# Optimization experiments

Hardware: AMD Instinct MI355X
Metric: run time of the kernel (lower is better)

The kernel has to match this reference:

```python
import jax, jax.numpy as jnp
import numpy as np

H = 1024   # longformer-large hidden size
D = 256    # transformer d_model / args.hidden_dim
Q = 100    # num_queries / num_slots
N = 1024   # document length (unpadded tokens)
L = 30     # args.max_span_length
WD = 20    # span width embedding dim
S = N * L - L * (L - 1) // 2  # 30285 candidate spans


def _ln(x, g, b, eps=1e-5):
    m = jnp.mean(x, -1, keepdims=True)
    v = jnp.mean((x - m) ** 2, -1, keepdims=True)
    return (x - m) * jax.lax.rsqrt(v + eps) * g + b


def setup_inputs():
    ks = jax.random.split(jax.random.key(0), 16)
    # deterministic span enumeration: triu(0) & tril(L-1) mention mask, row-major
    idx = np.arange(N)
    m = (idx[None, :] >= idx[:, None]) & (idx[None, :] < idx[:, None] + L)
    ss, ee = np.nonzero(m)
    assert ss.shape[0] == S
    r = lambda i, shape, s=0.02: jax.random.normal(ks[i], shape, jnp.float32) * s
    z = lambda *shape: jnp.zeros(shape, jnp.float32)
    o = lambda *shape: jnp.ones(shape, jnp.float32)
    return dict(
        encoded_doc=jax.random.normal(ks[0], (1, N, H), jnp.float32),
        span_starts=jnp.asarray(ss, jnp.int32),
        span_ends=jnp.asarray(ee, jnp.int32),
        w_word_attn=r(1, (H, 1)), b_word_attn=z(1),
        span_width_embed=r(2, (L, WD)),
        w_span_proj=r(3, (3 * H + WD, D)), b_span_proj=z(D),
        slots_query=r(4, (Q, D)),
        wq=r(5, (D, D)), bq=z(D),
        wk=r(6, (D, D)), bk=z(D),
        wv=r(7, (D, D)), bv=z(D),
        w_ih=r(8, (3 * D, D)), w_hh=r(9, (3 * D, D)), b_ih=z(3 * D), b_hh=z(3 * D),
        w_mlp1=r(10, (D, 2 * D)), b_mlp1=z(2 * D),
        w_mlp2=r(11, (2 * D, D)), b_mlp2=z(D),
        g_in=o(D), beta_in=z(D),
        g_sl=o(D), beta_sl=z(D),
        g_ff=o(D), beta_ff=z(D),
    )


def reference(encoded_doc, span_starts, span_ends, w_word_attn, b_word_attn,
              span_width_embed, w_span_proj, b_span_proj, slots_query,
              wq, bq, wk, bk, wv, bv, w_ih, w_hh, b_ih, b_hh,
              w_mlp1, b_mlp1, w_mlp2, b_mlp2,
              g_in, beta_in, g_sl, beta_sl, g_ff, beta_ff):
    doc = encoded_doc[0]                                   # [N, H]
    # --- get_span_emb ---
    start_emb = doc[span_starts]                           # [S, H]
    end_emb = doc[span_ends]                               # [S, H]
    width_idx = jnp.minimum(1 + span_ends - span_starts, L) - 1
    width_emb = span_width_embed[width_idx]                # [S, WD]
    word_attn = (doc @ w_word_attn)[:, 0] + b_word_attn[0] # [N]
    pos = jnp.arange(N)
    smask = (pos[None, :] >= span_starts[:, None]) & (pos[None, :] <= span_ends[:, None])
    scores = jnp.where(smask, word_attn[None, :], -jnp.inf)  # log(mask)+attn
    head = jax.nn.softmax(scores, axis=-1) @ doc           # [S, H]
    span_emb = jnp.concatenate([start_emb, end_emb, width_emb, head], -1)[None]  # [1,S,3H+WD]
    x = span_emb @ w_span_proj + b_span_proj               # [1, S, D]
    # --- slot attention ---
    inputs = _ln(x, g_in, beta_in)
    k = inputs @ wk + bk
    v = inputs @ wv + bv
    scale = D ** -0.5
    eps = 1e-8
    slots = slots_query[None]                              # [1, Q, D]
    for _ in range(3):
        slots_prev = slots
        q = _ln(slots, g_sl, beta_sl) @ wq + bq
        dots = jnp.einsum('bid,bjd->bij', q, k) * scale    # [1, Q, S]
        attn = jax.nn.softmax(dots, axis=1) + eps          # softmax over slots!
        attn = attn / jnp.sum(attn, -1, keepdims=True)
        updates = jnp.einsum('bjd,bij->bid', v, attn)      # [1, Q, D]
        # torch GRUCell
        xg = updates.reshape(-1, D)
        h = slots_prev.reshape(-1, D)
        gi = xg @ w_ih.T + b_ih
        gh = h @ w_hh.T + b_hh
        ir, iz, inn = jnp.split(gi, 3, -1)
        hr, hz, hn = jnp.split(gh, 3, -1)
        rg = jax.nn.sigmoid(ir + hr)
        zg = jax.nn.sigmoid(iz + hz)
        ng = jnp.tanh(inn + rg * hn)
        slots = ((1.0 - zg) * ng + zg * h).reshape(1, -1, D)
        ff = _ln(slots, g_ff, beta_ff)
        slots = slots + jax.nn.relu(ff @ w_mlp1 + b_mlp1) @ w_mlp2 + b_mlp2
    q = _ln(slots, g_sl, beta_sl) @ wq + bq
    dots = jnp.einsum('bid,bjd->bij', q, k) * scale
    coref_logits = jnp.minimum(jax.nn.softmax(dots, axis=1) + eps, 1.0)  # [1, Q, S]
    return coref_logits, inputs
```

## Files before the change

kernel.cpp:

```cpp
#include <hip/hip_runtime.h>

#define S_TOT 30285
#define SPAD  30720
#define EPS_S 3.0285e-4f

typedef __attribute__((ext_vector_type(8))) short bf16x8;
typedef __attribute__((ext_vector_type(4))) float f32x4;

__device__ __forceinline__ unsigned short f2bf(float f) {
  unsigned u = __float_as_uint(f);
  u += 0x7FFFu + ((u >> 16) & 1u);
  return (unsigned short)(u >> 16);
}
__device__ __forceinline__ float bf2f(unsigned short h) {
  return __uint_as_float(((unsigned)h) << 16);
}
__device__ __forceinline__ float allred_sum(float v) {
#pragma unroll
  for (int o = 32; o > 0; o >>= 1) v += __shfl_xor(v, o, 64);
  return v;
}

__global__ void k_prep(const float* __restrict__ doc, const float* __restrict__ w_wa,
                       const float* __restrict__ b_wa, const float* __restrict__ wemb,
                       const float* __restrict__ wsp, const float* __restrict__ wk,
                       const float* __restrict__ wv, const float* __restrict__ wq,
                       const float* __restrict__ w1, const float* __restrict__ w2,
                       const float* __restrict__ wih, const float* __restrict__ whh,
                       const float* __restrict__ slots_q, float* __restrict__ wa,
                       float* __restrict__ Wd, unsigned short* __restrict__ docb,
                       unsigned short* __restrict__ wihb, unsigned short* __restrict__ whhb,
                       unsigned short* __restrict__ wspT, unsigned short* __restrict__ wkT,
                       unsigned short* __restrict__ wvT, unsigned short* __restrict__ wqT,
                       unsigned short* __restrict__ w1T, unsigned short* __restrict__ w2T,
                       float* __restrict__ slots, float* __restrict__ zeroF,
                       unsigned short* __restrict__ inbpad) {
  __shared__ float shf[1056];
  int b = blockIdx.x, t = threadIdx.x;
  if (b < 1024) {
    float s = 0.f;
    for (int h = t; h < 1024; h += 256) s += doc[b * 1024 + h] * w_wa[h];
    shf[t] = s;
    __syncthreads();
    for (int o = 128; o; o >>= 1) {
      if (t < o) shf[t] += shf[t + o];
      __syncthreads();
    }
    if (t == 0) wa[b] = shf[0] + b_wa[0];
  } else if (b < 1054) {
    int w = b - 1024;
    float s = 0.f;
    for (int j = 0; j < 20; j++) s += wemb[w * 20 + j] * wsp[(2048 + j) * 256 + t];
    Wd[w * 256 + t] = s;
  } else if (b < 6686) {
    int b2 = b - 1054;
    if (b2 < 4096) { int i = b2 * 256 + t; docb[i] = f2bf(doc[i]); }
    else if (b2 < 4864) { int i = (b2 - 4096) * 256 + t; wihb[i] = f2bf(wih[i]); }
    else { int i = (b2 - 4864) * 256 + t; whhb[i] = f2bf(whh[i]); }
  } else if (b < 7902) {
    int bb = b - 6686;
    const float* src; unsigned short* dst; int R, C, tid;
    if (bb < 768) {
      int sec = bb >> 8; tid = bb & 255;
      src = wsp + (sec == 0 ? 0 : (sec == 1 ? 1024 * 256 : 2068 * 256));
      dst = wspT + (size_t)sec * 256 * 1024; R = 1024; C = 256;
    } else if (bb < 832) { src = wk; dst = wkT; R = 256; C = 256; tid = bb - 768; }
    else if (bb < 896) { src = wv; dst = wvT; R = 256; C = 256; tid = bb - 832; }
    else if (bb < 960) { src = wq; dst = wqT; R = 256; C = 256; tid = bb - 896; }
    else if (bb < 1088) { src = w1; dst = w1T; R = 256; C = 512; tid = bb - 960; }
    else { src = w2; dst = w2T; R = 512; C = 256; tid = bb - 1088; }
    int cw = C >> 5;
    int c0 = (tid % cw) * 32, r0 = (tid / cw) * 32;
#pragma unroll
    for (int i = 0; i < 4; i++) {
      int e = i * 256 + t, rr = e >> 5, cc = e & 31;
      shf[rr * 33 + cc] = src[(size_t)(r0 + rr) * C + c0 + cc];
    }
    __syncthreads();
#pragma unroll
    for (int i = 0; i < 4; i++) {
      int e = i * 256 + t, cc = e >> 5, rr = e & 31;
      dst[(size_t)(c0 + cc) * R + r0 + rr] = f2bf(shf[rr * 33 + cc]);
    }
  } else if (b < 7909) {
    int r0 = (b - 7902) * 16;
    for (int rr = 0; rr < 16; rr++) {
      int row = r0 + rr;
      slots[row * 256 + t] = (row < 100) ? slots_q[row * 256 + t] : 0.f;
    }
  } else if (b < 7994) {
    int i4 = (b - 7909) * 256 + t;
    if (i4 < 21664) ((float4*)zeroF)[i4] = (float4){0.f, 0.f, 0.f, 0.f};
  } else {
    int i = (b - 7994) * 256 + t;
    if (i < 13920) ((uint4*)inbpad)[i] = (uint4){0u, 0u, 0u, 0u};
  }
}

__global__ __launch_bounds__(256) void k_abc_mfma(const unsigned short* __restrict__ docb,
                                                  const unsigned short* __restrict__ wspT,
                                                  float* __restrict__ A, float* __restrict__ B,
                                                  float* __restrict__ C) {
  int rt = blockIdx.x, sec = blockIdx.y;
  float* out = sec == 0 ? A : (sec == 1 ? B : C);
  const unsigned short* wt = wspT + (size_t)sec * 256 * 1024;
  __shared__ unsigned short lds[64 * 256];
  int t = threadIdx.x, w = t >> 6, l = t & 63, lr = l & 15, lh = l >> 4;
  f32x4 acc[4][4];
#pragma unroll
  for (int m = 0; m < 4; m++)
#pragma unroll
    for (int n = 0; n < 4; n++) acc[m][n] = (f32x4){0.f, 0.f, 0.f, 0.f};
  for (int kt = 0; kt < 4; kt++) {
    __syncthreads();
#pragma unroll
    for (int it = 0; it < 8; it++) {
      int e = it * 256 + t, row = e >> 5, c16 = e & 31;
      int ba = ((row * 512) + c16 * 16) ^ ((row & 7) << 4);
      *(uint4*)((char*)lds + ba) =
          *(const uint4*)(docb + (size_t)(rt * 64 + row) * 1024 + kt * 256 + c16 * 8);
    }
    __syncthreads();
    for (int kk = 0; kk < 8; kk++) {
      bf16x8 afr[4];
#pragma unroll
      for (int m = 0; m < 4; m++) {
        int row = m * 16 + lr;
        int ba = ((row * 512) + kk * 64 + lh * 16) ^ ((row & 7) << 4);
        afr[m] = *(bf16x8*)((char*)lds + ba);
      }
#pragma unroll
      for (int n = 0; n < 4; n++) {
        bf16x8 b8 = *(const bf16x8*)(wt + (size_t)(w * 64 + n * 16 + lr) * 1024 + kt * 256 +
                                     kk * 32 + lh * 8);
#pragma unroll
        for (int m = 0; m < 4; m++)
          acc[m][n] = __builtin_amdgcn_mfma_f32_16x16x32_bf16(afr[m], b8, acc[m][n], 0, 0, 0);
      }
    }
  }
#pragma unroll
  for (int n = 0; n < 4; n++) {
    int col = w * 64 + n * 16 + lr;
#pragma unroll
    for (int m = 0; m < 4; m++)
#pragma unroll
      for (int r = 0; r < 4; r++)
        out[(size_t)(rt * 64 + m * 16 + lh * 4 + r) * 256 + col] = acc[m][n][r];
  }
}

__global__ void k_spans_ln(const float* __restrict__ wa, const float* __restrict__ A,
                           const float* __restrict__ B, const float* __restrict__ C,
                           const float* __restrict__ Wd, const float* __restrict__ bias,
                           const float* __restrict__ g_in, const float* __restrict__ be_in,
                           float* __restrict__ xin, unsigned short* __restrict__ inb) {
  int ss = blockIdx.x, t = threadIdx.x;
  int w = t >> 6, lane = t & 63;
  int nsp = min(30, 1024 - ss);
  int base = (ss < 995) ? ss * 30 : 29850 + 435 - ((1024 - ss) * (1025 - ss)) / 2;
  __shared__ float C_l[30 * 256];
  __shared__ float wa_l[30];
  for (int e = t; e < nsp * 256; e += 256)
    C_l[e] = C[(ss + (e >> 8)) * 256 + (e & 255)];
  if (t < nsp) wa_l[t] = wa[ss + t];
  __syncthreads();
  int c0 = lane * 4;
  float4 aS = *(const float4*)(A + ss * 256 + c0);
  float4 bi = *(const float4*)(bias + c0);
  float a0 = aS.x + bi.x, a1 = aS.y + bi.y, a2 = aS.z + bi.z, a3 = aS.w + bi.w;
  float4 gg = *(const float4*)(g_in + c0);
  float4 bb = *(const float4*)(be_in + c0);
  float m = -3.4e38f, Z = 0.f;
  float W0 = 0.f, W1 = 0.f, W2 = 0.f, W3 = 0.f;
  int pos = 0;
  for (int sp = w; sp < nsp; sp += 4) {
    for (; pos <= sp; ++pos) {
      float as_ = wa_l[pos];
      float mn = fmaxf(m, as_);
      float corr = __expf(m - mn);
      float e = __expf(as_ - mn);
      Z = Z * corr + e;
      float4 cc = *(const float4*)(C_l + pos * 256 + c0);
      W0 = W0 * corr + e * cc.x;
      W1 = W1 * corr + e * cc.y;
      W2 = W2 * corr + e * cc.z;
      W3 = W3 * corr + e * cc.w;
      m = mn;
    }
    float invZ = 1.f / Z;
    float4 Bv = *(const float4*)(B + (size_t)(ss + sp) * 256 + c0);
    float4 wd = *(const float4*)(Wd + sp * 256 + c0);
    float v0 = a0 + Bv.x + wd.x + W0 * invZ;
    float v1 = a1 + Bv.y + wd.y + W1 * invZ;
    float v2 = a2 + Bv.z + wd.z + W2 * invZ;
    float v3 = a3 + Bv.w + wd.w + W3 * invZ;
    float s = allred_sum(v0 + v1 + v2 + v3);
    float mean = s * (1.f / 256.f);
    float d0 = v0 - mean, d1 = v1 - mean, d2 = v2 - mean, d3 = v3 - mean;
    float q = allred_sum(d0 * d0 + d1 * d1 + d2 * d2 + d3 * d3);
    float rstd = rsqrtf(q * (1.f / 256.f) + 1e-5f);
    float o0 = d0 * rstd * gg.x + bb.x;
    float o1 = d1 * rstd * gg.y + bb.y;
    float o2 = d2 * rstd * gg.z + bb.z;
    float o3 = d3 * rstd * gg.w + bb.w;
    size_t r = (size_t)(base + sp) * 256 + c0;
    *(float4*)(xin + r) = (float4){o0, o1, o2, o3};
    ushort4 u4;
    u4.x = f2bf(o0); u4.y = f2bf(o1); u4.z = f2bf(o2); u4.w = f2bf(o3);
    *(ushort4*)(inb + r) = u4;
  }
}

__global__ __launch_bounds__(256) void k_kv_mfma(const unsigned short* __restrict__ inb,
                                                 const unsigned short* __restrict__ wkT,
                                                 const unsigned short* __restrict__ wvT,
                                                 const float* __restrict__ bk,
                                                 const float* __restrict__ bv,
                                                 unsigned short* __restrict__ kb,
                                                 unsigned short* __restrict__ vT,
                                                 float* __restrict__ vsum) {
  int j0 = blockIdx.x * 64;
  int t = threadIdx.x, w = t >> 6, l = t & 63, lr = l & 15, lh = l >> 4;
  __shared__ unsigned short lds[64 * 256];
#pragma unroll
  for (int it = 0; it < 8; it++) {
    int e = it * 256 + t, row = e >> 5, c16 = e & 31;
    int ba = ((row * 512) + c16 * 16) ^ ((row & 7) << 4);
    *(uint4*)((char*)lds + ba) = *(const uint4*)(inb + (size_t)(j0 + row) * 256 + c16 * 8);
  }
  __syncthreads();
  f32x4 ak[4][4], av[4][4];
#pragma unroll
  for (int m = 0; m < 4; m++)
#pragma unroll
    for (int n = 0; n < 4; n++) {
      ak[m][n] = (f32x4){0.f, 0.f, 0.f, 0.f};
      av[m][n] = (f32x4){0.f, 0.f, 0.f, 0.f};
    }
  for (int kk = 0; kk < 8; kk++) {
    bf16x8 afr[4];
#pragma unroll
    for (int m = 0; m < 4; m++) {
      int row = m * 16 + lr;
      int ba = ((row * 512) + kk * 64 + lh * 16) ^ ((row & 7) << 4);
      afr[m] = *(bf16x8*)((char*)lds + ba);
    }
#pragma unroll
    for (int n = 0; n < 4; n++) {
      int col = w * 64 + n * 16 + lr;
      bf16x8 bk8 = *(const bf16x8*)(wkT + (size_t)col * 256 + kk * 32 + lh * 8);
      bf16x8 bv8 = *(const bf16x8*)(wvT + (size_t)col * 256 + kk * 32 + lh * 8);
#pragma unroll
      for (int m = 0; m < 4; m++) {
        ak[m][n] = __builtin_amdgcn_mfma_f32_16x16x32_bf16(afr[m], bk8, ak[m][n], 0, 0, 0);
        av[m][n] = __builtin_amdgcn_mfma_f32_16x16x32_bf16(afr[m], bv8, av[m][n], 0, 0, 0);
      }
    }
  }
#pragma unroll
  for (int n = 0; n < 4; n++) {
    int col = w * 64 + n * 16 + lr;
    float bks = bk[col], bvs = bv[col];
    float cs = 0.f;
#pragma unroll
    for (int m = 0; m < 4; m++)
#pragma unroll
      for (int r = 0; r < 4; r++) {
        int row = j0 + m * 16 + lh * 4 + r;
        float kvv = ak[m][n][r] + bks;
        float vvv = av[m][n][r] + bvs;
        kb[(size_t)row * 256 + col] = f2bf(kvv);
        vT[(size_t)col * SPAD + row] = f2bf(vvv);
        if (row < S_TOT) cs += vvv;
      }
    cs += __shfl_xor(cs, 16, 64);
    cs += __shfl_xor(cs, 32, 64);
    if (lh == 0) atomicAdd(&vsum[col], cs);
  }
}

__global__ void k_qln0(const float* __restrict__ slots, const float* __restrict__ g_sl,
                       const float* __restrict__ be_sl, const unsigned short* __restrict__ wqT,
                       const float* __restrict__ bq, unsigned short* __restrict__ qbf) {
  int i = blockIdx.x, t = threadIdx.x;
  if (i >= 100) { qbf[i * 256 + t] = 0; return; }
  __shared__ float ln_l[256];
  __shared__ float red[8];
  int wave = t >> 6, lane = t & 63;
  float v = slots[i * 256 + t];
  float s = allred_sum(v);
  if (lane == 0) red[wave] = s;
  __syncthreads();
  float mean = (red[0] + red[1] + red[2] + red[3]) * (1.f / 256.f);
  float dv = v - mean;
  float s2 = allred_sum(dv * dv);
  if (lane == 0) red[4 + wave] = s2;
  __syncthreads();
  float var = (red[4] + red[5] + red[6] + red[7]) * (1.f / 256.f);
  ln_l[t] = dv * rsqrtf(var + 1e-5f) * g_sl[t] + be_sl[t];
  __syncthreads();
  float q = bq[t];
  size_t c = (size_t)t * 256;
  for (int d = 0; d < 256; d += 8) {
    bf16x8 a = *(const bf16x8*)(wqT + c + d);
#pragma unroll
    for (int e = 0; e < 8; e++) q += bf2f((unsigned short)a[e]) * ln_l[d + e];
  }
  qbf[i * 256 + t] = f2bf(q);
}

__global__ __launch_bounds__(256) void k_dots_f(const unsigned short* __restrict__ kb,
                                                const unsigned short* __restrict__ qb,
                                                unsigned short* __restrict__ pT,
                                                float* __restrict__ rowsum,
                                                float* __restrict__ coref, int final_, int S_) {
  int j0 = blockIdx.x * 64;
  int t = threadIdx.x, w = t >> 6, l = t & 63, lr = l & 15, lh = l >> 4;
  f32x4 acc[7];
#pragma unroll
  for (int n = 0; n < 7; n++) acc[n] = (f32x4){0.f, 0.f, 0.f, 0.f};
  const unsigned short* arow = kb + (size_t)(j0 + w * 16 + lr) * 256;
  for (int kk = 0; kk < 8; kk++) {
    bf16x8 a8 = *(const bf16x8*)(arow + kk * 32 + lh * 8);
#pragma unroll
    for (int n = 0; n < 7; n++) {
      bf16x8 b8 = *(const bf16x8*)(qb + (size_t)(n * 16 + lr) * 256 + kk * 32 + lh * 8);
      acc[n] = __builtin_amdgcn_mfma_f32_16x16x32_bf16(a8, b8, acc[n], 0, 0, 0);
    }
  }
  __shared__ float dt[64][117];
#pragma unroll
  for (int n = 0; n < 7; n++)
#pragma unroll
    for (int r = 0; r < 4; r++) dt[w * 16 + lh * 4 + r][n * 16 + lr] = acc[n][r] * 0.0625f;
  __syncthreads();
  int jj = t >> 2, q4 = t & 3;
  float mx = -3.4e38f;
#pragma unroll
  for (int i = 0; i < 25; i++) mx = fmaxf(mx, dt[jj][q4 * 25 + i]);
  mx = fmaxf(mx, __shfl_xor(mx, 1, 64));
  mx = fmaxf(mx, __shfl_xor(mx, 2, 64));
  float sm = 0.f;
#pragma unroll
  for (int i = 0; i < 25; i++) {
    float e = __expf(dt[jj][q4 * 25 + i] - mx);
    dt[jj][q4 * 25 + i] = e;
    sm += e;
  }
  sm += __shfl_xor(sm, 1, 64);
  sm += __shfl_xor(sm, 2, 64);
  float inv = 1.f / sm;
#pragma unroll
  for (int i = 0; i < 25; i++) dt[jj][q4 * 25 + i] *= inv;
  __syncthreads();
  if (!final_) {
    for (int e = t; e < 112 * 64; e += 256) {
      int i = e >> 6, j2 = e & 63;
      float pv = (i < 100 && (j0 + j2) < S_) ? dt[j2][i] : 0.f;
      pT[(size_t)i * SPAD + j0 + j2] = f2bf(pv);
    }
    int nv = S_ - j0;
    if (nv > 64) nv = 64;
    if (t < 100) {
      float s = 0.f;
      for (int j2 = 0; j2 < nv; j2++) s += dt[j2][t];
      atomicAdd(rowsum + t, s);
    }
  } else {
    for (int e = t; e < 100 * 64; e += 256) {
      int i = e >> 6, j2 = e & 63;
      if ((j0 + j2) < S_) coref[(size_t)i * S_ + j0 + j2] = fminf(dt[j2][i] + 1e-8f, 1.0f);
    }
  }
}

__global__ __launch_bounds__(256) void k_upd_mfma(const unsigned short* __restrict__ pT,
                                                  const unsigned short* __restrict__ vT,
                                                  float* __restrict__ uraw) {
  int kc = blockIdx.x, ny = blockIdx.y;
  int t = threadIdx.x, w = t >> 6, l = t & 63, lr = l & 15, lh = l >> 4;
  int k0 = kc * 320;
  int c0 = ny * 128 + w * 32;
  f32x4 acc[7][2];
#pragma unroll
  for (int m = 0; m < 7; m++) {
    acc[m][0] = (f32x4){0.f, 0.f, 0.f, 0.f};
    acc[m][1] = (f32x4){0.f, 0.f, 0.f, 0.f};
  }
  for (int ks = 0; ks < 10; ks++) {
    int kof = k0 + ks * 32 + lh * 8;
    bf16x8 b0 = *(const bf16x8*)(vT + (size_t)(c0 + lr) * SPAD + kof);
    bf16x8 b1 = *(const bf16x8*)(vT + (size_t)(c0 + 16 + lr) * SPAD + kof);
#pragma unroll
    for (int m = 0; m < 7; m++) {
      bf16x8 a8 = *(const bf16x8*)(pT + (size_t)(m * 16 + lr) * SPAD + kof);
      acc[m][0] = __builtin_amdgcn_mfma_f32_16x16x32_bf16(a8, b0, acc[m][0], 0, 0, 0);
      acc[m][1] = __builtin_amdgcn_mfma_f32_16x16x32_bf16(a8, b1, acc[m][1], 0, 0, 0);
    }
  }
#pragma unroll
  for (int m = 0; m < 7; m++)
#pragma unroll
    for (int n = 0; n < 2; n++)
#pragma unroll
      for (int r = 0; r < 4; r++) {
        int i = m * 16 + lh * 4 + r;
        if (i < 100) atomicAdd(&uraw[i * 256 + c0 + n * 16 + lr], acc[m][n][r]);
      }
}

__global__ __launch_bounds__(256) void k_slot_tail(
    const float* __restrict__ uraw, const float* __restrict__ vsum,
    const float* __restrict__ rs, float* __restrict__ slots,
    const unsigned short* __restrict__ wihb, const unsigned short* __restrict__ whhb,
    const float* __restrict__ b_ih, const float* __restrict__ b_hh,
    const unsigned short* __restrict__ w1T, const float* __restrict__ b1,
    const unsigned short* __restrict__ w2T, const float* __restrict__ b2,
    const float* __restrict__ g_ff, const float* __restrict__ be_ff,
    const float* __restrict__ g_sl, const float* __restrict__ be_sl,
    const unsigned short* __restrict__ wqT, const float* __restrict__ bq,
    unsigned short* __restrict__ qbf) {
  int i = blockIdx.x, t = threadIdx.x;
  if (i >= 100) { qbf[i * 256 + t] = 0; return; }
  __shared__ float u_l[256], h_l[256], sff[256], shid[512];
  __shared__ float red[8];
  int wave = t >> 6, lane = t & 63;
  float u = (uraw[i * 256 + t] + 1e-8f * vsum[t]) / (rs[i] + EPS_S);
  float h = slots[i * 256 + t];
  u_l[t] = u;
  h_l[t] = h;
  __syncthreads();
  float gA0 = b_ih[t], gA1 = b_ih[t + 256], gA2 = b_ih[t + 512];
  float gB0 = b_hh[t], gB1 = b_hh[t + 256], gB2 = b_hh[t + 512];
#pragma unroll
  for (int p = 0; p < 3; p++) {
    size_t c = (size_t)(t + p * 256) * 256;
    float si = 0.f, sh = 0.f;
    for (int d = 0; d < 256; d += 8) {
      bf16x8 a = *(const bf16x8*)(wihb + c + d);
      bf16x8 b = *(const bf16x8*)(whhb + c + d);
#pragma unroll
      for (int e = 0; e < 8; e++) {
        si += bf2f((unsigned short)a[e]) * u_l[d + e];
        sh += bf2f((unsigned short)b[e]) * h_l[d + e];
      }
    }
    if (p == 0) { gA0 += si; gB0 += sh; }
    else if (p == 1) { gA1 += si; gB1 += sh; }
    else { gA2 += si; gB2 += sh; }
  }
  float rg = 1.f / (1.f + __expf(-(gA0 + gB0)));
  float zg = 1.f / (1.f + __expf(-(gA1 + gB1)));
  float ng = tanhf(gA2 + rg * gB2);
  float ns_ = (1.f - zg) * ng + zg * h;
  float s = allred_sum(ns_);
  if (lane == 0) red[wave] = s;
  __syncthreads();
  float mean = (red[0] + red[1] + red[2] + red[3]) * (1.f / 256.f);
  float dv = ns_ - mean;
  float s2 = allred_sum(dv * dv);
  if (lane == 0) red[4 + wave] = s2;
  __syncthreads();
  float var = (red[4] + red[5] + red[6] + red[7]) * (1.f / 256.f);
  sff[t] = dv * rsqrtf(var + 1e-5f) * g_ff[t] + be_ff[t];
  __syncthreads();
  float h1 = b1[t], h2 = b1[t + 256];
  {
    size_t c1 = (size_t)t * 256, c2 = (size_t)(t + 256) * 256;
    for (int d = 0; d < 256; d += 8) {
      bf16x8 a = *(const bf16x8*)(w1T + c1 + d);
      bf16x8 b = *(const bf16x8*)(w1T + c2 + d);
#pragma unroll
      for (int e = 0; e < 8; e++) {
        float f = sff[d + e];
        h1 += bf2f((unsigned short)a[e]) * f;
        h2 += bf2f((unsigned short)b[e]) * f;
      }
    }
  }
  shid[t] = fmaxf(h1, 0.f);
  shid[t + 256] = fmaxf(h2, 0.f);
  __syncthreads();
  float o = ns_ + b2[t];
  {
    size_t c = (size_t)t * 512;
    for (int d = 0; d < 512; d += 8) {
      bf16x8 a = *(const bf16x8*)(w2T + c + d);
#pragma unroll
      for (int e = 0; e < 8; e++) o += bf2f((unsigned short)a[e]) * shid[d + e];
    }
  }
  slots[i * 256 + t] = o;
  float s3 = allred_sum(o);
  if (lane == 0) red[wave] = s3;
  __syncthreads();
  float mean2 = (red[0] + red[1] + red[2] + red[3]) * (1.f / 256.f);
  float dv2 = o - mean2;
  float s4 = allred_sum(dv2 * dv2);
  if (lane == 0) red[4 + wave] = s4;
  __syncthreads();
  float var2 = (red[4] + red[5] + red[6] + red[7]) * (1.f / 256.f);
  float lnq = dv2 * rsqrtf(var2 + 1e-5f) * g_sl[t] + be_sl[t];
  __syncthreads();
  u_l[t] = lnq;
  __syncthreads();
  float q = bq[t];
  {
    size_t c = (size_t)t * 256;
    for (int d = 0; d < 256; d += 8) {
      bf16x8 a = *(const bf16x8*)(wqT + c + d);
#pragma unroll
      for (int e = 0; e < 8; e++) q += bf2f((unsigned short)a[e]) * u_l[d + e];
    }
  }
  qbf[i * 256 + t] = f2bf(q);
}

extern "C" void kernel_launch(void* const* d_in, const int* in_sizes, int n_in,
                              void* d_out, int out_size, void* d_ws, size_t ws_size,
                              hipStream_t stream) {
  const float* doc = (const float*)d_in[0];
  const float* w_wa = (const float*)d_in[3];
  const float* b_wa = (const float*)d_in[4];
  const float* wemb = (const float*)d_in[5];
  const float* wsp = (const float*)d_in[6];
  const float* bsp = (const float*)d_in[7];
  const float* slots_q = (const float*)d_in[8];
  const float* wq = (const float*)d_in[9];
  const float* bq = (const float*)d_in[10];
  const float* wk = (const float*)d_in[11];
  const float* bk = (const float*)d_in[12];
  const float* wv = (const float*)d_in[13];
  const float* bv = (const float*)d_in[14];
  const float* w_ih = (const float*)d_in[15];
  const float* w_hh = (const float*)d_in[16];
  const float* b_ih = (const float*)d_in[17];
  const float* b_hh = (const float*)d_in[18];
  const float* w1 = (const float*)d_in[19];
  const float* b1 = (const float*)d_in[20];
  const float* w2 = (const float*)d_in[21];
  const float* b2 = (const float*)d_in[22];
  const float* g_in = (const float*)d_in[23];
  const float* be_in = (const float*)d_in[24];
  const float* g_sl = (const float*)d_in[25];
  const float* be_sl = (const float*)d_in[26];
  const float* g_ff = (const float*)d_in[27];
  const float* be_ff = (const float*)d_in[28];

  const int S = S_TOT;
  float* out = (float*)d_out;
  float* coref = out;
  float* xin = out + 100 * S;

  float* ws = (float*)d_ws;
  float* wa = ws;
  float* Wd = wa + 1024;
  float* A = Wd + 7680;
  float* Bm = A + 262144;
  float* Cm = Bm + 262144;
  float* vsum = Cm + 262144;
  float* rowsum = vsum + 256;
  float* uraw = rowsum + 384;
  float* slots = uraw + 86016;
  unsigned short* ub = (unsigned short*)(slots + 28672);
  unsigned short* inb = ub;
  unsigned short* kbuf = inb + (size_t)SPAD * 256;
  unsigned short* vT = kbuf + (size_t)SPAD * 256;
  unsigned short* pT = vT + (size_t)SPAD * 256;
  unsigned short* qbf = pT + (size_t)112 * SPAD;
  unsigned short* docb = qbf + 112 * 256;
  unsigned short* wspT = docb + 1024 * 1024;
  unsigned short* wkT = wspT + 768 * 1024;
  unsigned short* wvT = wkT + 256 * 256;
  unsigned short* wqT = wvT + 256 * 256;
  unsigned short* wihb = wqT + 256 * 256;
  unsigned short* whhb = wihb + 768 * 256;
  unsigned short* w1T = whhb + 768 * 256;
  unsigned short* w2T = w1T + 512 * 256;

  k_prep<<<8049, 256, 0, stream>>>(doc, w_wa, b_wa, wemb, wsp, wk, wv, wq, w1, w2,
                                   w_ih, w_hh, slots_q, wa, Wd, docb, wihb, whhb, wspT,
                                   wkT, wvT, wqT, w1T, w2T, slots, vsum,
                                   inb + (size_t)S * 256);
  k_abc_mfma<<<dim3(16, 3), 256, 0, stream>>>(docb, wspT, A, Bm, Cm);
  k_spans_ln<<<1024, 256, 0, stream>>>(wa, A, Bm, Cm, Wd, bsp, g_in, be_in, xin, inb);
  k_kv_mfma<<<SPAD / 64, 256, 0, stream>>>(inb, wkT, wvT, bk, bv, kbuf, vT, vsum);
  k_qln0<<<112, 256, 0, stream>>>(slots, g_sl, be_sl, wqT, bq, qbf);

  for (int it = 0; it < 3; ++it) {
    float* rs_it = rowsum + it * 128;
    float* uraw_it = uraw + it * 28672;
    k_dots_f<<<SPAD / 64, 256, 0, stream>>>(kbuf, qbf, pT, rs_it, coref, 0, S);
    k_upd_mfma<<<dim3(96, 2), 256, 0, stream>>>(pT, vT, uraw_it);
    k_slot_tail<<<112, 256, 0, stream>>>(uraw_it, vsum, rs_it, slots, wihb, whhb,
                                         b_ih, b_hh, w1T, b1, w2T, b2, g_ff, be_ff,
                                         g_sl, be_sl, wqT, bq, qbf);
  }
  k_dots_f<<<SPAD / 64, 256, 0, stream>>>(kbuf, qbf, pT, rowsum, coref, 1, S);
}
```

Before: 412.4 us.

## Rewrite slot-tail GRU/MLP/query projection as 16-row MFMA tiles

Replaces the per-slot scalar GRU, MLP and query-projection kernel (one block per slot, 112 blocks) with a kernel that processes 16 slots per block using bf16 MFMA instructions, launching 7 blocks. Activations are staged in swizzled LDS as bf16, and layernorm statistics use single-pass sum and sum of squares. The aim is to stop every block re-reading the full weight matrices from memory and to use matrix cores instead of scalar FMAs. In exchange, the GRU inputs and hidden states are rounded to bf16 before the matmuls, and only 7 CUs do the work.

```diff
diff --git a/kernel.cpp b/kernel.cpp
--- a/kernel.cpp
+++ b/kernel.cpp
@@ -410,7 +410,7 @@
       }
 }
 
-__global__ __launch_bounds__(256) void k_slot_tail(
+__global__ __launch_bounds__(256) void k_tail16(
     const float* __restrict__ uraw, const float* __restrict__ vsum,
     const float* __restrict__ rs, float* __restrict__ slots,
     const unsigned short* __restrict__ wihb, const unsigned short* __restrict__ whhb,
@@ -421,100 +421,244 @@
     const float* __restrict__ g_sl, const float* __restrict__ be_sl,
     const unsigned short* __restrict__ wqT, const float* __restrict__ bq,
     unsigned short* __restrict__ qbf) {
-  int i = blockIdx.x, t = threadIdx.x;
-  if (i >= 100) { qbf[i * 256 + t] = 0; return; }
-  __shared__ float u_l[256], h_l[256], sff[256], shid[512];
-  __shared__ float red[8];
-  int wave = t >> 6, lane = t & 63;
-  float u = (uraw[i * 256 + t] + 1e-8f * vsum[t]) / (rs[i] + EPS_S);
-  float h = slots[i * 256 + t];
-  u_l[t] = u;
-  h_l[t] = h;
-  __syncthreads();
-  float gA0 = b_ih[t], gA1 = b_ih[t + 256], gA2 = b_ih[t + 512];
-  float gB0 = b_hh[t], gB1 = b_hh[t + 256], gB2 = b_hh[t + 512];
-#pragma unroll
-  for (int p = 0; p < 3; p++) {
-    size_t c = (size_t)(t + p * 256) * 256;
-    float si = 0.f, sh = 0.f;
-    for (int d = 0; d < 256; d += 8) {
-      bf16x8 a = *(const bf16x8*)(wihb + c + d);
-      bf16x8 b = *(const bf16x8*)(whhb + c + d);
-#pragma unroll
-      for (int e = 0; e < 8; e++) {
-        si += bf2f((unsigned short)a[e]) * u_l[d + e];
-        sh += bf2f((unsigned short)b[e]) * h_l[d + e];
-      }
-    }
-    if (p == 0) { gA0 += si; gB0 += sh; }
-    else if (p == 1) { gA1 += si; gB1 += sh; }
-    else { gA2 += si; gB2 += sh; }
-  }
-  float rg = 1.f / (1.f + __expf(-(gA0 + gB0)));
-  float zg = 1.f / (1.f + __expf(-(gA1 + gB1)));
-  float ng = tanhf(gA2 + rg * gB2);
-  float ns_ = (1.f - zg) * ng + zg * h;
-  float s = allred_sum(ns_);
-  if (lane == 0) red[wave] = s;
-  __syncthreads();
-  float mean = (red[0] + red[1] + red[2] + red[3]) * (1.f / 256.f);
-  float dv = ns_ - mean;
-  float s2 = allred_sum(dv * dv);
-  if (lane == 0) red[4 + wave] = s2;
-  __syncthreads();
-  float var = (red[4] + red[5] + red[6] + red[7]) * (1.f / 256.f);
-  sff[t] = dv * rsqrtf(var + 1e-5f) * g_ff[t] + be_ff[t];
-  __syncthreads();
-  float h1 = b1[t], h2 = b1[t + 256];
+  int R0 = blockIdx.x * 16;
+  int t = threadIdx.x, w = t >> 6, l = t & 63, lr = l & 15, lh = l >> 4;
+  __shared__ unsigned short ub[16 * 256];
+  __shared__ unsigned short hb[16 * 256];
+  __shared__ float hfl[16 * 256];
+  __shared__ float nsl[16 * 256];
+  __shared__ unsigned short sfb[16 * 256];
+  __shared__ unsigned short hid[16 * 512];
+  __shared__ float stat[16][2];
+
+  for (int e = t; e < 16 * 32; e += 256) {
+    int row = e >> 5, c8 = (e & 31) * 8;
+    int rg = R0 + row;
+    float inv = 1.f / (rs[rg] + EPS_S);
+    float4 u0 = *(const float4*)(uraw + rg * 256 + c8);
+    float4 u1 = *(const float4*)(uraw + rg * 256 + c8 + 4);
+    float4 vs0 = *(const float4*)(vsum + c8);
+    float4 vs1 = *(const float4*)(vsum + c8 + 4);
+    float4 h0 = *(const float4*)(slots + rg * 256 + c8);
+    float4 h1 = *(const float4*)(slots + rg * 256 + c8 + 4);
+    bf16x8 au, ah;
+    au[0] = (short)f2bf((u0.x + 1e-8f * vs0.x) * inv);
+    au[1] = (short)f2bf((u0.y + 1e-8f * vs0.y) * inv);
+    au[2] = (short)f2bf((u0.z + 1e-8f * vs0.z) * inv);
+    au[3] = (short)f2bf((u0.w + 1e-8f * vs0.w) * inv);
+    au[4] = (short)f2bf((u1.x + 1e-8f * vs1.x) * inv);
+    au[5] = (short)f2bf((u1.y + 1e-8f * vs1.y) * inv);
+    au[6] = (short)f2bf((u1.z + 1e-8f * vs1.z) * inv);
+    au[7] = (short)f2bf((u1.w + 1e-8f * vs1.w) * inv);
+    ah[0] = (short)f2bf(h0.x); ah[1] = (short)f2bf(h0.y);
+    ah[2] = (short)f2bf(h0.z); ah[3] = (short)f2bf(h0.w);
+    ah[4] = (short)f2bf(h1.x); ah[5] = (short)f2bf(h1.y);
+    ah[6] = (short)f2bf(h1.z); ah[7] = (short)f2bf(h1.w);
+    int ba = (row * 512 + c8 * 2) ^ ((row & 7) << 4);
+    *(bf16x8*)((char*)ub + ba) = au;
+    *(bf16x8*)((char*)hb + ba) = ah;
+    *(float4*)(hfl + row * 256 + c8) = h0;
+    *(float4*)(hfl + row * 256 + c8 + 4) = h1;
+  }
+  __syncthreads();
+
   {
-    size_t c1 = (size_t)t * 256, c2 = (size_t)(t + 256) * 256;
-    for (int d = 0; d < 256; d += 8) {
-      bf16x8 a = *(const bf16x8*)(w1T + c1 + d);
-      bf16x8 b = *(const bf16x8*)(w1T + c2 + d);
-#pragma unroll
-      for (int e = 0; e < 8; e++) {
-        float f = sff[d + e];
-        h1 += bf2f((unsigned short)a[e]) * f;
-        h2 += bf2f((unsigned short)b[e]) * f;
-      }
-    }
-  }
-  shid[t] = fmaxf(h1, 0.f);
-  shid[t + 256] = fmaxf(h2, 0.f);
-  __syncthreads();
-  float o = ns_ + b2[t];
+    f32x4 ai[12], ah2[12];
+#pragma unroll
+    for (int j = 0; j < 12; j++) {
+      ai[j] = (f32x4){0.f, 0.f, 0.f, 0.f};
+      ah2[j] = (f32x4){0.f, 0.f, 0.f, 0.f};
+    }
+    for (int kk = 0; kk < 8; kk++) {
+      int ka = (lr * 512 + kk * 64 + lh * 16) ^ ((lr & 7) << 4);
+      bf16x8 a8u = *(bf16x8*)((char*)ub + ka);
+      bf16x8 a8h = *(bf16x8*)((char*)hb + ka);
+      int d0 = kk * 32 + lh * 8;
+#pragma unroll
+      for (int j = 0; j < 12; j++) {
+        int c0 = 16 * (w + 4 * j);
+        bf16x8 bi8 = *(const bf16x8*)(wihb + (size_t)(c0 + lr) * 256 + d0);
+        bf16x8 bh8 = *(const bf16x8*)(whhb + (size_t)(c0 + lr) * 256 + d0);
+        ai[j] = __builtin_amdgcn_mfma_f32_16x16x32_bf16(a8u, bi8, ai[j], 0, 0, 0);
+        ah2[j] = __builtin_amdgcn_mfma_f32_16x16x32_bf16(a8h, bh8, ah2[j], 0, 0, 0);
+      }
+    }
+#pragma unroll
+    for (int j = 0; j < 4; j++) {
+      int col = 16 * (w + 4 * j) + lr;
+      float bi0 = b_ih[col], bi1 = b_ih[col + 256], bi2 = b_ih[col + 512];
+      float bh0 = b_hh[col], bh1 = b_hh[col + 256], bh2 = b_hh[col + 512];
+#pragma unroll
+      for (int r = 0; r < 4; r++) {
+        int row = lh * 4 + r;
+        float ir = ai[j][r] + bi0, iz = ai[j + 4][r] + bi1, inn = ai[j + 8][r] + bi2;
+        float hr = ah2[j][r] + bh0, hz = ah2[j + 4][r] + bh1, hn = ah2[j + 8][r] + bh2;
+        float rg = 1.f / (1.f + __expf(-(ir + hr)));
+        float zg = 1.f / (1.f + __expf(-(iz + hz)));
+        float ng = tanhf(inn + rg * hn);
+        nsl[row * 256 + col] = (1.f - zg) * ng + zg * hfl[row * 256 + col];
+      }
+    }
+  }
+  __syncthreads();
+
+#pragma unroll
+  for (int rr = 0; rr < 4; rr++) {
+    int row = w * 4 + rr;
+    float4 v = *(const float4*)(nsl + row * 256 + l * 4);
+    float s = allred_sum(v.x + v.y + v.z + v.w);
+    float q = allred_sum(v.x * v.x + v.y * v.y + v.z * v.z + v.w * v.w);
+    if (l == 0) {
+      float mean = s * (1.f / 256.f);
+      float var = fmaxf(q * (1.f / 256.f) - mean * mean, 0.f);
+      stat[row][0] = mean;
+      stat[row][1] = rsqrtf(var + 1e-5f);
+    }
+  }
+  __syncthreads();
+  for (int e = t; e < 16 * 32; e += 256) {
+    int row = e >> 5, c8 = (e & 31) * 8;
+    float mean = stat[row][0], rstd = stat[row][1];
+    float4 g0 = *(const float4*)(g_ff + c8), g1 = *(const float4*)(g_ff + c8 + 4);
+    float4 e0 = *(const float4*)(be_ff + c8), e1 = *(const float4*)(be_ff + c8 + 4);
+    float4 n0 = *(const float4*)(nsl + row * 256 + c8);
+    float4 n1 = *(const float4*)(nsl + row * 256 + c8 + 4);
+    bf16x8 a;
+    a[0] = (short)f2bf((n0.x - mean) * rstd * g0.x + e0.x);
+    a[1] = (short)f2bf((n0.y - mean) * rstd * g0.y + e0.y);
+    a[2] = (short)f2bf((n0.z - mean) * rstd * g0.z + e0.z);
+    a[3] = (short)f2bf((n0.w - mean) * rstd * g0.w + e0.w);
+    a[4] = (short)f2bf((n1.x - mean) * rstd * g1.x + e1.x);
+    a[5] = (short)f2bf((n1.y - mean) * rstd * g1.y + e1.y);
+    a[6] = (short)f2bf((n1.z - mean) * rstd * g1.z + e1.z);
+    a[7] = (short)f2bf((n1.w - mean) * rstd * g1.w + e1.w);
+    int ba = (row * 512 + c8 * 2) ^ ((row & 7) << 4);
+    *(bf16x8*)((char*)sfb + ba) = a;
+  }
+  __syncthreads();
+
   {
-    size_t c = (size_t)t * 512;
-    for (int d = 0; d < 512; d += 8) {
-      bf16x8 a = *(const bf16x8*)(w2T + c + d);
-#pragma unroll
-      for (int e = 0; e < 8; e++) o += bf2f((unsigned short)a[e]) * shid[d + e];
-    }
-  }
-  slots[i * 256 + t] = o;
-  float s3 = allred_sum(o);
-  if (lane == 0) red[wave] = s3;
-  __syncthreads();
-  float mean2 = (red[0] + red[1] + red[2] + red[3]) * (1.f / 256.f);
-  float dv2 = o - mean2;
-  float s4 = allred_sum(dv2 * dv2);
-  if (lane == 0) red[4 + wave] = s4;
-  __syncthreads();
-  float var2 = (red[4] + red[5] + red[6] + red[7]) * (1.f / 256.f);
-  float lnq = dv2 * rsqrtf(var2 + 1e-5f) * g_sl[t] + be_sl[t];
-  __syncthreads();
-  u_l[t] = lnq;
-  __syncthreads();
-  float q = bq[t];
+    f32x4 m1[8];
+#pragma unroll
+    for (int j = 0; j < 8; j++) m1[j] = (f32x4){0.f, 0.f, 0.f, 0.f};
+    for (int kk = 0; kk < 8; kk++) {
+      int ka = (lr * 512 + kk * 64 + lh * 16) ^ ((lr & 7) << 4);
+      bf16x8 a8 = *(bf16x8*)((char*)sfb + ka);
+      int d0 = kk * 32 + lh * 8;
+#pragma unroll
+      for (int j = 0; j < 8; j++) {
+        int c0 = 16 * (w * 8 + j);
+        bf16x8 b8 = *(const bf16x8*)(w1T + (size_t)(c0 + lr) * 256 + d0);
+        m1[j] = __builtin_amdgcn_mfma_f32_16x16x32_bf16(a8, b8, m1[j], 0, 0, 0);
+      }
+    }
+#pragma unroll
+    for (int j = 0; j < 8; j++) {
+      int col = 16 * (w * 8 + j) + lr;
+      float bb = b1[col];
+#pragma unroll
+      for (int r = 0; r < 4; r++) {
+        int row = lh * 4 + r;
+        int ba = (row * 1024 + col * 2) ^ ((row & 7) << 4);
+        *(unsigned short*)((char*)hid + ba) = f2bf(fmaxf(m1[j][r] + bb, 0.f));
+      }
+    }
+  }
+  __syncthreads();
+
   {
-    size_t c = (size_t)t * 256;
-    for (int d = 0; d < 256; d += 8) {
-      bf16x8 a = *(const bf16x8*)(wqT + c + d);
-#pragma unroll
-      for (int e = 0; e < 8; e++) q += bf2f((unsigned short)a[e]) * u_l[d + e];
-    }
-  }
-  qbf[i * 256 + t] = f2bf(q);
+    f32x4 m2[4];
+#pragma unroll
+    for (int j = 0; j < 4; j++) m2[j] = (f32x4){0.f, 0.f, 0.f, 0.f};
+    for (int kk = 0; kk < 16; kk++) {
+      int ka = (lr * 1024 + kk * 64 + lh * 16) ^ ((lr & 7) << 4);
+      bf16x8 a8 = *(bf16x8*)((char*)hid + ka);
+      int d0 = kk * 32 + lh * 8;
+#pragma unroll
+      for (int j = 0; j < 4; j++) {
+        int c0 = 16 * (w * 4 + j);
+        bf16x8 b8 = *(const bf16x8*)(w2T + (size_t)(c0 + lr) * 512 + d0);
+        m2[j] = __builtin_amdgcn_mfma_f32_16x16x32_bf16(a8, b8, m2[j], 0, 0, 0);
+      }
+    }
+#pragma unroll
+    for (int j = 0; j < 4; j++) {
+      int col = 16 * (w * 4 + j) + lr;
+      float bb = b2[col];
+#pragma unroll
+      for (int r = 0; r < 4; r++) {
+        int row = lh * 4 + r;
+        float o = m2[j][r] + bb + nsl[row * 256 + col];
+        hfl[row * 256 + col] = o;
+        int rg = R0 + row;
+        if (rg < 100) slots[rg * 256 + col] = o;
+      }
+    }
+  }
+  __syncthreads();
+
+#pragma unroll
+  for (int rr = 0; rr < 4; rr++) {
+    int row = w * 4 + rr;
+    float4 v = *(const float4*)(hfl + row * 256 + l * 4);
+    float s = allred_sum(v.x + v.y + v.z + v.w);
+    float q = allred_sum(v.x * v.x + v.y * v.y + v.z * v.z + v.w * v.w);
+    if (l == 0) {
+      float mean = s * (1.f / 256.f);
+      float var = fmaxf(q * (1.f / 256.f) - mean * mean, 0.f);
+      stat[row][0] = mean;
+      stat[row][1] = rsqrtf(var + 1e-5f);
+    }
+  }
+  __syncthreads();
+  for (int e = t; e < 16 * 32; e += 256) {
+    int row = e >> 5, c8 = (e & 31) * 8;
+    float mean = stat[row][0], rstd = stat[row][1];
+    float4 g0 = *(const float4*)(g_sl + c8), g1 = *(const float4*)(g_sl + c8 + 4);
+    float4 e0 = *(const float4*)(be_sl + c8), e1 = *(const float4*)(be_sl + c8 + 4);
+    float4 n0 = *(const float4*)(hfl + row * 256 + c8);
+    float4 n1 = *(const float4*)(hfl + row * 256 + c8 + 4);
+    bf16x8 a;
+    a[0] = (short)f2bf((n0.x - mean) * rstd * g0.x + e0.x);
+    a[1] = (short)f2bf((n0.y - mean) * rstd * g0.y + e0.y);
+    a[2] = (short)f2bf((n0.z - mean) * rstd * g0.z + e0.z);
+    a[3] = (short)f2bf((n0.w - mean) * rstd * g0.w + e0.w);
+    a[4] = (short)f2bf((n1.x - mean) * rstd * g1.x + e1.x);
+    a[5] = (short)f2bf((n1.y - mean) * rstd * g1.y + e1.y);
+    a[6] = (short)f2bf((n1.z - mean) * rstd * g1.z + e1.z);
+    a[7] = (short)f2bf((n1.w - mean) * rstd * g1.w + e1.w);
+    int ba = (row * 512 + c8 * 2) ^ ((row & 7) << 4);
+    *(bf16x8*)((char*)sfb + ba) = a;
+  }
+  __syncthreads();
+
+  {
+    f32x4 mq[4];
+#pragma unroll
+    for (int j = 0; j < 4; j++) mq[j] = (f32x4){0.f, 0.f, 0.f, 0.f};
+    for (int kk = 0; kk < 8; kk++) {
+      int ka = (lr * 512 + kk * 64 + lh * 16) ^ ((lr & 7) << 4);
+      bf16x8 a8 = *(bf16x8*)((char*)sfb + ka);
+      int d0 = kk * 32 + lh * 8;
+#pragma unroll
+      for (int j = 0; j < 4; j++) {
+        int c0 = 16 * (w * 4 + j);
+        bf16x8 b8 = *(const bf16x8*)(wqT + (size_t)(c0 + lr) * 256 + d0);
+        mq[j] = __builtin_amdgcn_mfma_f32_16x16x32_bf16(a8, b8, mq[j], 0, 0, 0);
+      }
+    }
+#pragma unroll
+    for (int j = 0; j < 4; j++) {
+      int col = 16 * (w * 4 + j) + lr;
+      float bb = bq[col];
+#pragma unroll
+      for (int r = 0; r < 4; r++) {
+        int row = lh * 4 + r;
+        int rg = R0 + row;
+        qbf[(size_t)rg * 256 + col] = (rg < 100) ? f2bf(mq[j][r] + bb) : (unsigned short)0;
+      }
+    }
+  }
 }
 
 extern "C" void kernel_launch(void* const* d_in, const int* in_sizes, int n_in,
@@ -593,9 +737,9 @@
     float* uraw_it = uraw + it * 28672;
     k_dots_f<<<SPAD / 64, 256, 0, stream>>>(kbuf, qbf, pT, rs_it, coref, 0, S);
     k_upd_mfma<<<dim3(96, 2), 256, 0, stream>>>(pT, vT, uraw_it);
-    k_slot_tail<<<112, 256, 0, stream>>>(uraw_it, vsum, rs_it, slots, wihb, whhb,
-                                         b_ih, b_hh, w1T, b1, w2T, b2, g_ff, be_ff,
-                                         g_sl, be_sl, wqT, bq, qbf);
+    k_tail16<<<7, 256, 0, stream>>>(uraw_it, vsum, rs_it, slots, wihb, whhb,
+                                    b_ih, b_hh, w1T, b1, w2T, b2, g_ff, be_ff,
+                                    g_sl, be_sl, wqT, bq, qbf);
   }
   k_dots_f<<<SPAD / 64, 256, 0, stream>>>(kbuf, qbf, pT, rowsum, coref, 1, S);
 }
```

After: 450.9 us. +9.3%, slower.

## Stage GRU and MLP weights through double-buffered LDS with split-K GEMV in slot tail

Applied to the files above, without the earlier changes.

Replaces the per-thread row dot products in the slot update kernel, where each thread walked its own weight row with strided global loads, with a cooperative scheme. The block loads 8192-element weight chunks into a double-buffered, padded shared-memory tile with coalesced loads and prefetches the next chunk while computing. It then does a split-K dot product with shuffle reductions. The grid also shrinks to exactly 100 blocks, dropping the padding blocks that rewrote zero query rows, and it relies on those rows already being zero from the initial query kernel. This adds extra barriers and about 33KB of shared memory per block.

```diff
diff --git a/kernel.cpp b/kernel.cpp
--- a/kernel.cpp
+++ b/kernel.cpp
@@ -410,6 +410,90 @@
       }
 }
 
+
+#define WBUF_EL 8448
+
+__device__ __forceinline__ void gemv_g256(const unsigned short* __restrict__ W, int nchunks,
+                                          const float* __restrict__ xl, float* __restrict__ outp,
+                                          unsigned short* __restrict__ wbuf, int t) {
+  __syncthreads();
+  int s = t & 7, r = t >> 3;
+  float xseg[32];
+#pragma unroll
+  for (int k = 0; k < 8; k++) *(float4*)&xseg[k * 4] = *(const float4*)&xl[s * 32 + k * 4];
+  bf16x8 pf[4];
+#pragma unroll
+  for (int q = 0; q < 4; q++) pf[q] = *(const bf16x8*)(W + (size_t)(q * 256 + t) * 8);
+  for (int n = 0; n < nchunks; n++) {
+    unsigned short* buf = wbuf + (n & 1) * WBUF_EL;
+#pragma unroll
+    for (int q = 0; q < 4; q++) {
+      int idx = q * 256 + t;
+      *(bf16x8*)(buf + (idx >> 5) * 264 + (idx & 31) * 8) = pf[q];
+    }
+    if (n + 1 < nchunks) {
+      const unsigned short* src = W + (size_t)(n + 1) * 8192;
+#pragma unroll
+      for (int q = 0; q < 4; q++) pf[q] = *(const bf16x8*)(src + (size_t)(q * 256 + t) * 8);
+    }
+    __syncthreads();
+    const unsigned short* row = wbuf + (n & 1) * WBUF_EL + r * 264 + s * 32;
+    float acc = 0.f;
+#pragma unroll
+    for (int k8 = 0; k8 < 4; k8++) {
+      bf16x8 a = *(const bf16x8*)(row + k8 * 8);
+#pragma unroll
+      for (int e = 0; e < 8; e++) acc += bf2f((unsigned short)a[e]) * xseg[k8 * 8 + e];
+    }
+    acc += __shfl_xor(acc, 1, 64);
+    acc += __shfl_xor(acc, 2, 64);
+    acc += __shfl_xor(acc, 4, 64);
+    if (s == 0) outp[n * 32 + r] = acc;
+  }
+  __syncthreads();
+}
+
+__device__ __forceinline__ void gemv_g512(const unsigned short* __restrict__ W, int nchunks,
+                                          const float* __restrict__ xl, float* __restrict__ outp,
+                                          unsigned short* __restrict__ wbuf, int t) {
+  __syncthreads();
+  int s = t & 15, r = t >> 4;
+  float xseg[32];
+#pragma unroll
+  for (int k = 0; k < 8; k++) *(float4*)&xseg[k * 4] = *(const float4*)&xl[s * 32 + k * 4];
+  bf16x8 pf[4];
+#pragma unroll
+  for (int q = 0; q < 4; q++) pf[q] = *(const bf16x8*)(W + (size_t)(q * 256 + t) * 8);
+  for (int n = 0; n < nchunks; n++) {
+    unsigned short* buf = wbuf + (n & 1) * WBUF_EL;
+#pragma unroll
+    for (int q = 0; q < 4; q++) {
+      int idx = q * 256 + t;
+      *(bf16x8*)(buf + (idx >> 6) * 520 + (idx & 63) * 8) = pf[q];
+    }
+    if (n + 1 < nchunks) {
+      const unsigned short* src = W + (size_t)(n + 1) * 8192;
+#pragma unroll
+      for (int q = 0; q < 4; q++) pf[q] = *(const bf16x8*)(src + (size_t)(q * 256 + t) * 8);
+    }
+    __syncthreads();
+    const unsigned short* row = wbuf + (n & 1) * WBUF_EL + r * 520 + s * 32;
+    float acc = 0.f;
+#pragma unroll
+    for (int k8 = 0; k8 < 4; k8++) {
+      bf16x8 a = *(const bf16x8*)(row + k8 * 8);
+#pragma unroll
+      for (int e = 0; e < 8; e++) acc += bf2f((unsigned short)a[e]) * xseg[k8 * 8 + e];
+    }
+    acc += __shfl_xor(acc, 1, 64);
+    acc += __shfl_xor(acc, 2, 64);
+    acc += __shfl_xor(acc, 4, 64);
+    acc += __shfl_xor(acc, 8, 64);
+    if (s == 0) outp[n * 16 + r] = acc;
+  }
+  __syncthreads();
+}
+
 __global__ __launch_bounds__(256) void k_slot_tail(
     const float* __restrict__ uraw, const float* __restrict__ vsum,
     const float* __restrict__ rs, float* __restrict__ slots,
@@ -422,34 +506,23 @@
     const unsigned short* __restrict__ wqT, const float* __restrict__ bq,
     unsigned short* __restrict__ qbf) {
   int i = blockIdx.x, t = threadIdx.x;
-  if (i >= 100) { qbf[i * 256 + t] = 0; return; }
-  __shared__ float u_l[256], h_l[256], sff[256], shid[512];
+  __shared__ float u_l[256], h_l[256], shid[512];
+  __shared__ float gacc[1536];
+  __shared__ unsigned short wbuf[2 * WBUF_EL];
   __shared__ float red[8];
   int wave = t >> 6, lane = t & 63;
   float u = (uraw[i * 256 + t] + 1e-8f * vsum[t]) / (rs[i] + EPS_S);
   float h = slots[i * 256 + t];
   u_l[t] = u;
   h_l[t] = h;
-  __syncthreads();
-  float gA0 = b_ih[t], gA1 = b_ih[t + 256], gA2 = b_ih[t + 512];
-  float gB0 = b_hh[t], gB1 = b_hh[t + 256], gB2 = b_hh[t + 512];
-#pragma unroll
-  for (int p = 0; p < 3; p++) {
-    size_t c = (size_t)(t + p * 256) * 256;
-    float si = 0.f, sh = 0.f;
-    for (int d = 0; d < 256; d += 8) {
-      bf16x8 a = *(const bf16x8*)(wihb + c + d);
-      bf16x8 b = *(const bf16x8*)(whhb + c + d);
-#pragma unroll
-      for (int e = 0; e < 8; e++) {
-        si += bf2f((unsigned short)a[e]) * u_l[d + e];
-        sh += bf2f((unsigned short)b[e]) * h_l[d + e];
-      }
-    }
-    if (p == 0) { gA0 += si; gB0 += sh; }
-    else if (p == 1) { gA1 += si; gB1 += sh; }
-    else { gA2 += si; gB2 += sh; }
-  }
+  gemv_g256(wihb, 24, u_l, gacc, wbuf, t);
+  gemv_g256(whhb, 24, h_l, gacc + 768, wbuf, t);
+  float gA0 = gacc[t] + b_ih[t];
+  float gA1 = gacc[256 + t] + b_ih[t + 256];
+  float gA2 = gacc[512 + t] + b_ih[t + 512];
+  float gB0 = gacc[768 + t] + b_hh[t];
+  float gB1 = gacc[1024 + t] + b_hh[t + 256];
+  float gB2 = gacc[1280 + t] + b_hh[t + 512];
   float rg = 1.f / (1.f + __expf(-(gA0 + gB0)));
   float zg = 1.f / (1.f + __expf(-(gA1 + gB1)));
   float ng = tanhf(gA2 + rg * gB2);
@@ -463,34 +536,12 @@
   if (lane == 0) red[4 + wave] = s2;
   __syncthreads();
   float var = (red[4] + red[5] + red[6] + red[7]) * (1.f / 256.f);
-  sff[t] = dv * rsqrtf(var + 1e-5f) * g_ff[t] + be_ff[t];
-  __syncthreads();
-  float h1 = b1[t], h2 = b1[t + 256];
-  {
-    size_t c1 = (size_t)t * 256, c2 = (size_t)(t + 256) * 256;
-    for (int d = 0; d < 256; d += 8) {
-      bf16x8 a = *(const bf16x8*)(w1T + c1 + d);
-      bf16x8 b = *(const bf16x8*)(w1T + c2 + d);
-#pragma unroll
-      for (int e = 0; e < 8; e++) {
-        float f = sff[d + e];
-        h1 += bf2f((unsigned short)a[e]) * f;
-        h2 += bf2f((unsigned short)b[e]) * f;
-      }
-    }
-  }
-  shid[t] = fmaxf(h1, 0.f);
-  shid[t + 256] = fmaxf(h2, 0.f);
-  __syncthreads();
-  float o = ns_ + b2[t];
-  {
-    size_t c = (size_t)t * 512;
-    for (int d = 0; d < 512; d += 8) {
-      bf16x8 a = *(const bf16x8*)(w2T + c + d);
-#pragma unroll
-      for (int e = 0; e < 8; e++) o += bf2f((unsigned short)a[e]) * shid[d + e];
-    }
-  }
+  u_l[t] = dv * rsqrtf(var + 1e-5f) * g_ff[t] + be_ff[t];
+  gemv_g256(w1T, 16, u_l, gacc, wbuf, t);
+  shid[t] = fmaxf(gacc[t] + b1[t], 0.f);
+  shid[t + 256] = fmaxf(gacc[t + 256] + b1[t + 256], 0.f);
+  gemv_g512(w2T, 16, shid, gacc, wbuf, t);
+  float o = ns_ + b2[t] + gacc[t];
   slots[i * 256 + t] = o;
   float s3 = allred_sum(o);
   if (lane == 0) red[wave] = s3;
@@ -501,20 +552,9 @@
   if (lane == 0) red[4 + wave] = s4;
   __syncthreads();
   float var2 = (red[4] + red[5] + red[6] + red[7]) * (1.f / 256.f);
-  float lnq = dv2 * rsqrtf(var2 + 1e-5f) * g_sl[t] + be_sl[t];
-  __syncthreads();
-  u_l[t] = lnq;
-  __syncthreads();
-  float q = bq[t];
-  {
-    size_t c = (size_t)t * 256;
-    for (int d = 0; d < 256; d += 8) {
-      bf16x8 a = *(const bf16x8*)(wqT + c + d);
-#pragma unroll
-      for (int e = 0; e < 8; e++) q += bf2f((unsigned short)a[e]) * u_l[d + e];
-    }
-  }
-  qbf[i * 256 + t] = f2bf(q);
+  h_l[t] = dv2 * rsqrtf(var2 + 1e-5f) * g_sl[t] + be_sl[t];
+  gemv_g256(wqT, 8, h_l, gacc, wbuf, t);
+  qbf[i * 256 + t] = f2bf(bq[t] + gacc[t]);
 }
 
 extern "C" void kernel_launch(void* const* d_in, const int* in_sizes, int n_in,
@@ -593,7 +633,7 @@
     float* uraw_it = uraw + it * 28672;
     k_dots_f<<<SPAD / 64, 256, 0, stream>>>(kbuf, qbf, pT, rs_it, coref, 0, S);
     k_upd_mfma<<<dim3(96, 2), 256, 0, stream>>>(pT, vT, uraw_it);
-    k_slot_tail<<<112, 256, 0, stream>>>(uraw_it, vsum, rs_it, slots, wihb, whhb,
+    k_slot_tail<<<100, 256, 0, stream>>>(uraw_it, vsum, rs_it, slots, wihb, whhb,
                                          b_ih, b_hh, w1T, b1, w2T, b2, g_ff, be_ff,
                                          g_sl, be_sl, wqT, bq, qbf);
   }
```

Measured after the change: 408.2 us. No clear change (-1.0%).
